# Optimization experiments

Hardware: AMD Instinct MI355X
Metric: run time of the kernel (lower is better)

## Reference

```python
import jax, jax.numpy as jnp
import numpy as np


def _linear_params(key, fan_in, fan_out):
    # torch nn.Linear default init: U(-1/sqrt(fan_in), 1/sqrt(fan_in))
    kw, kb = jax.random.split(key)
    bound = 1.0 / np.sqrt(fan_in)
    W = jax.random.uniform(kw, (fan_out, fan_in), jnp.float32, -bound, bound)
    b = jax.random.uniform(kb, (fan_out,), jnp.float32, -bound, bound)
    return W, b


def setup_inputs() -> dict:
    key = jax.random.key(0)
    kx, k1, k7, k8, k9 = jax.random.split(key, 5)
    x = jax.random.normal(kx, (4194304, 6), dtype=jnp.float32)
    W1, b1 = _linear_params(k1, 6, 8)
    W7, b7 = _linear_params(k7, 8, 4)
    W8, b8 = _linear_params(k8, 4, 2)
    W9, b9 = _linear_params(k9, 2, 1)
    return {"x": x, "W1": W1, "b1": b1, "W7": W7, "b7": b7,
            "W8": W8, "b8": b8, "W9": W9, "b9": b9}


def reference(x, W1, b1, W7, b7, W8, b8, W9, b9):
    # forward only uses l1 -> relu -> l7 -> relu -> l8 -> relu -> l9 -> softplus
    z = jax.nn.relu(x @ W1.T + b1)      # [N, 8]
    z = jax.nn.relu(z @ W7.T + b7)      # [N, 4]
    z = jax.nn.relu(z @ W8.T + b8)      # [N, 2]
    z = z @ W9.T + b9                   # [N, 1]
    return jax.nn.softplus(z)
```

## Files before the change

kernel.cpp:

```cpp
#include <hip/hip_runtime.h>
#include <math.h>


typedef float v4f __attribute__((ext_vector_type(4)));

__device__ __forceinline__ float softplus_fast(float z) {
    float e = __expf(-fabsf(z));
    return fmaxf(z, 0.0f) + __logf(1.0f + e);
}

__device__ __forceinline__ void load_quad(const v4f* __restrict__ xin,
                                          size_t q, v4f b[6]) {
    const v4f* p = xin + q * 6;
    b[0] = p[0]; b[1] = p[1]; b[2] = p[2];
    b[3] = p[3]; b[4] = p[4]; b[5] = p[5];
}

__device__ __forceinline__ v4f compute_quad(
    const v4f b[6],
    const float* __restrict__ W1, const float* __restrict__ b1,
    const float* __restrict__ W7, const float* __restrict__ b7,
    const float* __restrict__ W8, const float* __restrict__ b8,
    const float* __restrict__ W9, const float* __restrict__ b9)
{
    float xr[4][6];
    xr[0][0]=b[0].x; xr[0][1]=b[0].y; xr[0][2]=b[0].z; xr[0][3]=b[0].w; xr[0][4]=b[1].x; xr[0][5]=b[1].y;
    xr[1][0]=b[1].z; xr[1][1]=b[1].w; xr[1][2]=b[2].x; xr[1][3]=b[2].y; xr[1][4]=b[2].z; xr[1][5]=b[2].w;
    xr[2][0]=b[3].x; xr[2][1]=b[3].y; xr[2][2]=b[3].z; xr[2][3]=b[3].w; xr[2][4]=b[4].x; xr[2][5]=b[4].y;
    xr[3][0]=b[4].z; xr[3][1]=b[4].w; xr[3][2]=b[5].x; xr[3][3]=b[5].y; xr[3][4]=b[5].z; xr[3][5]=b[5].w;

    v4f res;
    float out4[4];
    #pragma unroll
    for (int r = 0; r < 4; ++r) {
        float h1[8];
        #pragma unroll
        for (int j = 0; j < 8; ++j) {
            float acc = b1[j];
            #pragma unroll
            for (int k = 0; k < 6; ++k) acc = fmaf(W1[j * 6 + k], xr[r][k], acc);
            h1[j] = fmaxf(acc, 0.0f);
        }
        float h7[4];
        #pragma unroll
        for (int j = 0; j < 4; ++j) {
            float acc = b7[j];
            #pragma unroll
            for (int k = 0; k < 8; ++k) acc = fmaf(W7[j * 8 + k], h1[k], acc);
            h7[j] = fmaxf(acc, 0.0f);
        }
        float h8[2];
        #pragma unroll
        for (int j = 0; j < 2; ++j) {
            float acc = b8[j];
            #pragma unroll
            for (int k = 0; k < 4; ++k) acc = fmaf(W8[j * 4 + k], h7[k], acc);
            h8[j] = fmaxf(acc, 0.0f);
        }
        float z = fmaf(W9[0], h8[0], fmaf(W9[1], h8[1], b9[0]));
        out4[r] = softplus_fast(z);
    }
    res.x = out4[0]; res.y = out4[1]; res.z = out4[2]; res.w = out4[3];
    return res;
}

__global__ __launch_bounds__(256) void encoder_mlp_kernel(
    const float* __restrict__ x,
    const float* __restrict__ W1, const float* __restrict__ b1,
    const float* __restrict__ W7, const float* __restrict__ b7,
    const float* __restrict__ W8, const float* __restrict__ b8,
    const float* __restrict__ W9, const float* __restrict__ b9,
    float* __restrict__ out, int n_quads)
{
    const int t = blockIdx.x * blockDim.x + threadIdx.x;
    const size_t nthreads = (size_t)gridDim.x * blockDim.x;
    const v4f* xin = reinterpret_cast<const v4f*>(x);
    v4f* outv = reinterpret_cast<v4f*>(out);

    size_t q0 = (size_t)t;
    size_t q1 = q0 + nthreads;
    size_t q2 = q1 + nthreads;
    size_t q3 = q2 + nthreads;

    v4f bufA[6], bufB[6];

    if (q0 < (size_t)n_quads) load_quad(xin, q0, bufA);
    if (q1 < (size_t)n_quads) load_quad(xin, q1, bufB);

    if (q0 < (size_t)n_quads)
        outv[q0] = compute_quad(bufA, W1, b1, W7, b7, W8, b8, W9, b9);

    if (q2 < (size_t)n_quads) load_quad(xin, q2, bufA);
    if (q1 < (size_t)n_quads)
        outv[q1] = compute_quad(bufB, W1, b1, W7, b7, W8, b8, W9, b9);

    if (q3 < (size_t)n_quads) load_quad(xin, q3, bufB);
    if (q2 < (size_t)n_quads)
        outv[q2] = compute_quad(bufA, W1, b1, W7, b7, W8, b8, W9, b9);

    if (q3 < (size_t)n_quads)
        outv[q3] = compute_quad(bufB, W1, b1, W7, b7, W8, b8, W9, b9);
}

extern "C" void kernel_launch(void* const* d_in, const int* in_sizes, int n_in,
                              void* d_out, int out_size, void* d_ws, size_t ws_size,
                              hipStream_t stream) {
    const float* x  = (const float*)d_in[0];
    const float* W1 = (const float*)d_in[1];
    const float* b1 = (const float*)d_in[2];
    const float* W7 = (const float*)d_in[3];
    const float* b7 = (const float*)d_in[4];
    const float* W8 = (const float*)d_in[5];
    const float* b8 = (const float*)d_in[6];
    const float* W9 = (const float*)d_in[7];
    const float* b9 = (const float*)d_in[8];
    float* out = (float*)d_out;

    const int n_rows  = in_sizes[0] / 6;
    const int n_quads = (n_rows + 3) / 4;

    const int block = 256;
    const int quads_per_thread = 4;
    const int n_threads = (n_quads + quads_per_thread - 1) / quads_per_thread;
    const int grid = (n_threads + block - 1) / block;

    encoder_mlp_kernel<<<grid, block, 0, stream>>>(
        x, W1, b1, W7, b7, W8, b8, W9, b9, out, n_quads);
}
```

Baseline: 28.16 us.

## Stage input through LDS with direct global_load_lds, one quad per thread

Each wave now copies a contiguous 384-float4 tile of the input into shared memory with global_load_lds, using fully coalesced lane-strided 16-byte loads, then reads its own six float4s back from LDS. This replaces the strided per-thread 96-byte loads and the 4-quad software pipeline. The grid grows to one quad per thread, which trades the manual double-buffering for more waves in flight. Partial tiles fall back to a scalar, bounds-checked load path.

```diff
diff --git a/kernel.cpp b/kernel.cpp
--- a/kernel.cpp
+++ b/kernel.cpp
@@ -4,16 +4,12 @@
 
 typedef float v4f __attribute__((ext_vector_type(4)));
 
+#define AS1 __attribute__((address_space(1)))
+#define AS3 __attribute__((address_space(3)))
+
 __device__ __forceinline__ float softplus_fast(float z) {
     float e = __expf(-fabsf(z));
     return fmaxf(z, 0.0f) + __logf(1.0f + e);
-}
-
-__device__ __forceinline__ void load_quad(const v4f* __restrict__ xin,
-                                          size_t q, v4f b[6]) {
-    const v4f* p = xin + q * 6;
-    b[0] = p[0]; b[1] = p[1]; b[2] = p[2];
-    b[3] = p[3]; b[4] = p[4]; b[5] = p[5];
 }
 
 __device__ __forceinline__ v4f compute_quad(
@@ -29,7 +25,6 @@
     xr[2][0]=b[3].x; xr[2][1]=b[3].y; xr[2][2]=b[3].z; xr[2][3]=b[3].w; xr[2][4]=b[4].x; xr[2][5]=b[4].y;
     xr[3][0]=b[4].z; xr[3][1]=b[4].w; xr[3][2]=b[5].x; xr[3][3]=b[5].y; xr[3][4]=b[5].z; xr[3][5]=b[5].w;
 
-    v4f res;
     float out4[4];
     #pragma unroll
     for (int r = 0; r < 4; ++r) {
@@ -60,7 +55,7 @@
         float z = fmaf(W9[0], h8[0], fmaf(W9[1], h8[1], b9[0]));
         out4[r] = softplus_fast(z);
     }
-    res.x = out4[0]; res.y = out4[1]; res.z = out4[2]; res.w = out4[3];
+    v4f res; res.x = out4[0]; res.y = out4[1]; res.z = out4[2]; res.w = out4[3];
     return res;
 }
 
@@ -72,34 +67,59 @@
     const float* __restrict__ W9, const float* __restrict__ b9,
     float* __restrict__ out, int n_quads)
 {
-    const int t = blockIdx.x * blockDim.x + threadIdx.x;
-    const size_t nthreads = (size_t)gridDim.x * blockDim.x;
-    const v4f* xin = reinterpret_cast<const v4f*>(x);
-    v4f* outv = reinterpret_cast<v4f*>(out);
+    __shared__ v4f lds[4 * 384];
 
-    size_t q0 = (size_t)t;
-    size_t q1 = q0 + nthreads;
-    size_t q2 = q1 + nthreads;
-    size_t q3 = q2 + nthreads;
+    const int tid  = threadIdx.x;
+    const int wave = tid >> 6;
+    const int lane = tid & 63;
 
-    v4f bufA[6], bufB[6];
+    const int t = blockIdx.x * 256 + tid;
+    const size_t wave_tile = ((size_t)blockIdx.x * 4 + wave) * 384;
+    const size_t n_f4 = (size_t)n_quads * 6;
 
-    if (q0 < (size_t)n_quads) load_quad(xin, q0, bufA);
-    if (q1 < (size_t)n_quads) load_quad(xin, q1, bufB);
+    const v4f* x4 = reinterpret_cast<const v4f*>(x);
+    v4f* out4 = reinterpret_cast<v4f*>(out);
 
-    if (q0 < (size_t)n_quads)
-        outv[q0] = compute_quad(bufA, W1, b1, W7, b7, W8, b8, W9, b9);
+    const bool full_tile = (wave_tile + 384 <= n_f4);
 
-    if (q2 < (size_t)n_quads) load_quad(xin, q2, bufA);
-    if (q1 < (size_t)n_quads)
-        outv[q1] = compute_quad(bufB, W1, b1, W7, b7, W8, b8, W9, b9);
+    v4f r[6];
+    bool have_quad = ((size_t)t < (size_t)n_quads);
 
-    if (q3 < (size_t)n_quads) load_quad(xin, q3, bufB);
-    if (q2 < (size_t)n_quads)
-        outv[q2] = compute_quad(bufA, W1, b1, W7, b7, W8, b8, W9, b9);
+    if (full_tile) {
+        v4f* ldsw = &lds[wave * 384];
+        #pragma unroll
+        for (int j = 0; j < 6; ++j) {
+            const v4f* gp = x4 + wave_tile + (size_t)j * 64 + lane;
+            __builtin_amdgcn_global_load_lds(
+                (AS1 const unsigned int*)gp,
+                (AS3 unsigned int*)(ldsw + j * 64),
+                16, 0, 0);
+        }
+        asm volatile("s_waitcnt vmcnt(0)" ::: "memory");
+        __builtin_amdgcn_sched_barrier(0);
+        const v4f* my = &ldsw[lane * 6];
+        r[0] = my[0]; r[1] = my[1]; r[2] = my[2];
+        r[3] = my[3]; r[4] = my[4]; r[5] = my[5];
+    } else if (have_quad) {
+        const long long row0 = (long long)t * 4;
+        float tmp[24];
+        #pragma unroll
+        for (int q = 0; q < 4; ++q) {
+            long long row = row0 + q;
+            #pragma unroll
+            for (int k = 0; k < 6; ++k)
+                tmp[q * 6 + k] = (row * 6 + k < (long long)n_quads * 24)
+                                     ? x[row * 6 + k] : 0.0f;
+        }
+        #pragma unroll
+        for (int j = 0; j < 6; ++j) {
+            r[j].x = tmp[j*4+0]; r[j].y = tmp[j*4+1];
+            r[j].z = tmp[j*4+2]; r[j].w = tmp[j*4+3];
+        }
+    }
 
-    if (q3 < (size_t)n_quads)
-        outv[q3] = compute_quad(bufB, W1, b1, W7, b7, W8, b8, W9, b9);
+    if (have_quad)
+        out4[t] = compute_quad(r, W1, b1, W7, b7, W8, b8, W9, b9);
 }
 
 extern "C" void kernel_launch(void* const* d_in, const int* in_sizes, int n_in,
@@ -118,11 +138,8 @@
 
     const int n_rows  = in_sizes[0] / 6;
     const int n_quads = (n_rows + 3) / 4;
-
     const int block = 256;
-    const int quads_per_thread = 4;
-    const int n_threads = (n_quads + quads_per_thread - 1) / quads_per_thread;
-    const int grid = (n_threads + block - 1) / block;
+    const int grid = (n_quads + block - 1) / block;
 
     encoder_mlp_kernel<<<grid, block, 0, stream>>>(
         x, W1, b1, W7, b7, W8, b8, W9, b9, out, n_quads);
```

Result: no change. 28.31 us (+0.5%).
